# Kernel optimization log

Hardware: AMD Instinct MI355X
Metric: run time of the kernel (lower is better)

## Reference

```python
import jax, jax.numpy as jnp
import numpy as np

NEG_INF = -1e32

def _linear(x, W, b):
    # torch nn.Linear: x @ W.T + b
    return x @ W.T + b

def setup_inputs() -> dict:
    key = jax.random.key(0)
    B, T, D, H = 8, 1024, 512, 8
    ks = jax.random.split(key, 16)
    def rn(i, shape, scale=1.0):
        return jax.random.normal(ks[i], shape, dtype=jnp.float32) * scale
    W_SCALE = 0.04  # ~xavier for 512x512
    inp = {
        'q_mean': rn(0, (B, T, D)), 'q_cov': rn(1, (B, T, D)),
        'k_mean': rn(2, (B, T, D)), 'k_cov': rn(3, (B, T, D)),
        'v_mean': rn(4, (B, T, D)), 'v_cov': rn(5, (B, T, D)),
        # kq_same=True: q projections share k weights
        'Wk_mean': rn(6, (D, D), W_SCALE), 'bk_mean': jnp.zeros((D,), jnp.float32),
        'Wk_cov':  rn(7, (D, D), W_SCALE), 'bk_cov':  jnp.zeros((D,), jnp.float32),
        'Wv_mean': rn(8, (D, D), W_SCALE), 'bv_mean': jnp.zeros((D,), jnp.float32),
        'Wv_cov':  rn(9, (D, D), W_SCALE), 'bv_cov':  jnp.zeros((D,), jnp.float32),
        'Wo_mean': rn(10, (D, D), W_SCALE), 'bo_mean': jnp.zeros((D,), jnp.float32),
        'Wo_cov':  rn(11, (D, D), W_SCALE), 'bo_cov':  jnp.zeros((D,), jnp.float32),
        'gammas': rn(12, (H, 1, 1), 0.3),
        'mask': jnp.broadcast_to(jnp.tril(jnp.ones((T, T), dtype=bool))[None, None], (B, 1, T, T)),
        'zero_pad': 1,
    }
    return inp

def reference(q_mean, q_cov, k_mean, k_cov, v_mean, v_cov,
              Wk_mean, bk_mean, Wk_cov, bk_cov,
              Wv_mean, bv_mean, Wv_cov, bv_cov,
              Wo_mean, bo_mean, Wo_cov, bo_cov,
              gammas, mask, zero_pad):
    B, T, D = q_mean.shape
    H = gammas.shape[0]
    dk = D // H
    def split(x):  # (B,T,D) -> (B,H,T,dk)
        return x.reshape(B, T, H, dk).transpose(0, 2, 1, 3)
    km = split(_linear(k_mean, Wk_mean, bk_mean))
    kc = split(_linear(k_cov,  Wk_cov,  bk_cov))
    qm = split(_linear(q_mean, Wk_mean, bk_mean))  # kq_same
    qc = split(_linear(q_cov,  Wk_cov,  bk_cov))
    vm = split(_linear(v_mean, Wv_mean, bv_mean))
    vc = split(_linear(v_cov,  Wv_cov,  bv_cov))

    # Wasserstein distance (B,H,T,T)
    m1sq = jnp.sum(qm ** 2, -1, keepdims=True)
    m2sq = jnp.sum(km ** 2, -1, keepdims=True)
    ret = -2.0 * jnp.einsum('bhtd,bhsd->bhts', qm, km) + m1sq + jnp.swapaxes(m2sq, -1, -2)
    sq_q = jnp.sqrt(jnp.clip(qc, 1e-24))
    sq_k = jnp.sqrt(jnp.clip(kc, 1e-24))
    cov_ret = (-2.0 * jnp.einsum('bhtd,bhsd->bhts', sq_q, sq_k)
               + jnp.sum(qc, -1, keepdims=True)
               + jnp.swapaxes(jnp.sum(kc, -1, keepdims=True), -1, -2))
    scores = -(ret + cov_ret) / jnp.sqrt(jnp.float32(dk))

    # cumulative position-decay term (no-grad block in torch)
    s_ = jnp.where(mask, scores, NEG_INF)
    s_ = jax.nn.softmax(s_, axis=-1) * mask.astype(scores.dtype)
    distcum = jnp.cumsum(s_, axis=-1)
    disttot = jnp.sum(s_, axis=-1, keepdims=True)
    idx = jnp.arange(T)
    pos = jnp.abs(idx[None, :] - idx[:, None]).astype(jnp.float32)[None, None]  # (1,1,T,T)
    dist_scores = jax.lax.stop_gradient(jnp.sqrt(jnp.clip((disttot - distcum) * pos, 0.0)))

    gamma = -jax.nn.softplus(gammas)[None]  # (1,H,1,1)
    total_effect = jnp.clip(jnp.exp(dist_scores * gamma), 1e-5, 1e5)
    scores = jnp.where(mask, scores * total_effect, NEG_INF)
    scores = jax.nn.softmax(scores, axis=-1)
    if zero_pad:
        scores = scores.at[:, :, 0, :].set(0.0)
    # dropout is identity (p=0 / eval)

    out_mean = jnp.einsum('bhts,bhsd->bhtd', scores, vm)
    out_cov  = jnp.einsum('bhts,bhsd->bhtd', scores ** 2, vc)
    cm = out_mean.transpose(0, 2, 1, 3).reshape(B, T, D)
    cc = out_cov.transpose(0, 2, 1, 3).reshape(B, T, D)
    return (_linear(cm, Wo_mean, bo_mean), _linear(cc, Wo_cov, bo_cov))
```

## Files before the change

### kernel.cpp

```cpp
#include <hip/hip_runtime.h>
#include <hip/hip_bf16.h>
#include <hip/hip_fp16.h>

#define Bb 8
#define Tt 1024
#define Dd 512
#define Hh 8

typedef _Float16 half8 __attribute__((ext_vector_type(8)));
typedef float floatx4 __attribute__((ext_vector_type(4)));

__device__ __forceinline__ half8 cvt8(float4 a, float4 b) {
    half8 h;
    h[0] = (_Float16)a.x; h[1] = (_Float16)a.y; h[2] = (_Float16)a.z; h[3] = (_Float16)a.w;
    h[4] = (_Float16)b.x; h[5] = (_Float16)b.y; h[6] = (_Float16)b.z; h[7] = (_Float16)b.w;
    return h;
}

__device__ __forceinline__ void async16(const _Float16* g, _Float16* l) {
    __builtin_amdgcn_global_load_lds(
        (const __attribute__((address_space(1))) uint32_t*)g,
        (__attribute__((address_space(3))) uint32_t*)l, 16, 0, 0);
}

#define DPP_ADD(v, ctrl) \
    ((v) + __int_as_float(__builtin_amdgcn_update_dpp(0, __float_as_int(v), (ctrl), 0xF, 0xF, true)))

__device__ __forceinline__ float red16(float v) {
    v = DPP_ADD(v, 0xB1);
    v = DPP_ADD(v, 0x4E);
    v = DPP_ADD(v, 0x141);
    v = DPP_ADD(v, 0x140);
    return v;
}
__device__ __forceinline__ float scan16(float v) {
    v = DPP_ADD(v, 0x111);
    v = DPP_ADD(v, 0x112);
    v = DPP_ADD(v, 0x114);
    v = DPP_ADD(v, 0x118);
    return v;
}

template<bool TR>
__device__ __forceinline__ void gemm_tile(
    const float* __restrict__ X, const float* __restrict__ W,
    _Float16* As, _Float16* Bs, int m0, int n0, floatx4 acc[8])
{
    const int tid = threadIdx.x;
    const int w = tid >> 6, lane = tid & 63;
    const int sl = lane & 15, quad = lane >> 4;

    for (int k0 = 0; k0 < 512; k0 += 64) {
        __syncthreads();
        {
            const int r = tid >> 2;
            const int cb = (tid & 3) * 16;
            const float* xp = X + (size_t)(m0 + r) * 512 + k0 + cb;
            #pragma unroll
            for (int i = 0; i < 2; i++) {
                float4 v0 = *(const float4*)(xp + i * 8);
                float4 v1 = *(const float4*)(xp + i * 8 + 4);
                *(half8*)(As + r * 72 + cb + i * 8) = cvt8(v0, v1);
            }
        }
        {
            const int r = tid >> 1;
            const int cb = (tid & 1) * 32;
            const float* wp = W + (size_t)(n0 + r) * 512 + k0 + cb;
            #pragma unroll
            for (int i = 0; i < 4; i++) {
                float4 v0 = *(const float4*)(wp + i * 8);
                float4 v1 = *(const float4*)(wp + i * 8 + 4);
                *(half8*)(Bs + r * 72 + cb + i * 8) = cvt8(v0, v1);
            }
        }
        __syncthreads();
        #pragma unroll
        for (int kc = 0; kc < 64; kc += 32) {
            const half8 af = *(const half8*)(As + (w * 16 + sl) * 72 + kc + quad * 8);
            #pragma unroll
            for (int tn = 0; tn < 8; tn++) {
                const half8 bf = *(const half8*)(Bs + (tn * 16 + sl) * 72 + kc + quad * 8);
                if constexpr (TR)
                    acc[tn] = __builtin_amdgcn_mfma_f32_16x16x32_f16(bf, af, acc[tn], 0, 0, 0);
                else
                    acc[tn] = __builtin_amdgcn_mfma_f32_16x16x32_f16(af, bf, acc[tn], 0, 0, 0);
            }
        }
    }
}

__global__ __launch_bounds__(256) void gemm6(
    const float* __restrict__ q_mean, const float* __restrict__ q_cov,
    const float* __restrict__ k_mean, const float* __restrict__ k_cov,
    const float* __restrict__ v_mean, const float* __restrict__ v_cov,
    const float* __restrict__ Wk_mean, const float* __restrict__ bk_mean,
    const float* __restrict__ Wk_cov,  const float* __restrict__ bk_cov,
    const float* __restrict__ Wv_mean, const float* __restrict__ bv_mean,
    const float* __restrict__ Wv_cov,  const float* __restrict__ bv_cov,
    _Float16* __restrict__ QB, _Float16* __restrict__ KB, _Float16* __restrict__ VB,
    float* __restrict__ RROW, float* __restrict__ CCOL)
{
    __shared__ __align__(16) _Float16 As[64 * 72];
    __shared__ __align__(16) _Float16 Bs[128 * 72];

    const int f = blockIdx.x;
    const int work = (f & 7) * 384 + (f >> 3);
    const int z = work >> 9;
    const int rem = work & 511;
    const int m0 = (rem >> 2) * 64;
    const int n0 = (rem & 3) * 128;

    const float *X, *W, *bias; _Float16* outH; float* sums;
    int off, sumsq, do_sqrt;
    switch (z) {
    case 0:  X=q_mean; W=Wk_mean; bias=bk_mean; outH=QB; sums=RROW;   off=0;  sumsq=1; do_sqrt=0; break;
    case 1:  X=q_cov;  W=Wk_cov;  bias=bk_cov;  outH=QB; sums=RROW;   off=64; sumsq=0; do_sqrt=1; break;
    case 2:  X=k_mean; W=Wk_mean; bias=bk_mean; outH=KB; sums=CCOL;   off=0;  sumsq=1; do_sqrt=0; break;
    case 3:  X=k_cov;  W=Wk_cov;  bias=bk_cov;  outH=KB; sums=CCOL;   off=64; sumsq=0; do_sqrt=1; break;
    case 4:  X=v_mean; W=Wv_mean; bias=bv_mean; outH=VB; sums=nullptr;off=0;  sumsq=0; do_sqrt=0; break;
    default: X=v_cov;  W=Wv_cov;  bias=bv_cov;  outH=VB; sums=nullptr;off=64; sumsq=0; do_sqrt=0; break;
    }

    floatx4 acc[8];
    #pragma unroll
    for (int tn = 0; tn < 8; tn++) acc[tn] = (floatx4){0.f, 0.f, 0.f, 0.f};

    const int tid = threadIdx.x;
    const int w = tid >> 6, lane = tid & 63;
    const int sl = lane & 15, quad = lane >> 4;

    if (z < 4) {
        gemm_tile<false>(X, W, As, Bs, m0, n0, acc);
        #pragma unroll
        for (int r = 0; r < 4; r++) {
            const int m = m0 + w * 16 + quad * 4 + r;
            const int b = m >> 10, t = m & 1023;
            float rs0 = 0.f, rs1 = 0.f;
            #pragma unroll
            for (int tn = 0; tn < 8; tn++) {
                const int n = n0 + tn * 16 + sl;
                const float v = acc[tn][r] + bias[n];
                if (tn < 4) rs0 += sumsq ? v * v : v;
                else        rs1 += sumsq ? v * v : v;
                const float sv = do_sqrt ? sqrtf(fmaxf(v, 1e-24f)) : v;
                const int head = n >> 6, dd = n & 63;
                outH[(((size_t)b * Hh + head) * Tt + t) * 128 + off + dd] = (_Float16)sv;
            }
            if (sums) {
                float v0 = rs0, v1 = rs1;
                v0 += __shfl_xor(v0, 1); v0 += __shfl_xor(v0, 2);
                v0 += __shfl_xor(v0, 4); v0 += __shfl_xor(v0, 8);
                v1 += __shfl_xor(v1, 1); v1 += __shfl_xor(v1, 2);
                v1 += __shfl_xor(v1, 4); v1 += __shfl_xor(v1, 8);
                if (sl == 0) {
                    atomicAdd(&sums[((size_t)b * Hh + (n0 >> 6) + 0) * Tt + t], v0);
                    atomicAdd(&sums[((size_t)b * Hh + (n0 >> 6) + 1) * Tt + t], v1);
                }
            }
        }
    } else {
        gemm_tile<true>(X, W, As, Bs, m0, n0, acc);
        const int m = m0 + w * 16 + sl;
        const int b = m >> 10, t = m & 1023;
        #pragma unroll
        for (int r = 0; r < 4; r++) {
            #pragma unroll
            for (int tn = 0; tn < 8; tn++) {
                const int n = n0 + tn * 16 + quad * 4 + r;
                const float v = acc[tn][r] + bias[n];
                const int head = n >> 6, dd = n & 63;
                outH[(((size_t)b * Hh + head) * 128 + off + dd) * 1024 + t] = (_Float16)v;
            }
        }
    }
}

__global__ __launch_bounds__(256) void gemm_out(
    const float* __restrict__ CM, const float* __restrict__ CC,
    const float* __restrict__ Wo_mean, const float* __restrict__ bo_mean,
    const float* __restrict__ Wo_cov,  const float* __restrict__ bo_cov,
    float* __restrict__ out, size_t outStride)
{
    __shared__ __align__(16) _Float16 As[64 * 72];
    __shared__ __align__(16) _Float16 Bs[128 * 72];

    const int f = blockIdx.x;
    const int work = (f & 7) * 128 + (f >> 3);
    const int z = work >> 9;
    const int rem = work & 511;
    const int m0 = (rem >> 2) * 64;
    const int n0 = (rem & 3) * 128;

    const float* X    = z ? CC      : CM;
    const float* W    = z ? Wo_cov  : Wo_mean;
    const float* bias = z ? bo_cov  : bo_mean;
    float* outF       = out + (size_t)z * outStride;

    floatx4 acc[8];
    #pragma unroll
    for (int tn = 0; tn < 8; tn++) acc[tn] = (floatx4){0.f, 0.f, 0.f, 0.f};
    gemm_tile<false>(X, W, As, Bs, m0, n0, acc);

    const int tid = threadIdx.x;
    const int w = tid >> 6, lane = tid & 63;
    const int sl = lane & 15, quad = lane >> 4;

    #pragma unroll
    for (int r = 0; r < 4; r++) {
        const int m = m0 + w * 16 + quad * 4 + r;
        #pragma unroll
        for (int tn = 0; tn < 8; tn++) {
            const int n = n0 + tn * 16 + sl;
            outF[(size_t)m * 512 + n] = acc[tn][r] + bias[n];
        }
    }
}

__global__ __launch_bounds__(256) void attn_kernel(
    const _Float16* __restrict__ QB, const _Float16* __restrict__ KB,
    const _Float16* __restrict__ VBt, const float* __restrict__ RROW,
    const float* __restrict__ CCOL, const float* __restrict__ gammas,
    const int* __restrict__ zp, float* __restrict__ CM, float* __restrict__ CC)
{
    __shared__ __align__(16) _Float16 Vt[2][128 * 64];
    __shared__ __align__(16) _Float16 Pm[4][16 * 64];

    const int tid = threadIdx.x;
    const int g = blockIdx.x >> 6;
    const int bh = blockIdx.x & 63;
    const int rt = (g < 8) ? (15 - g) : (g - 8);
    const int t0 = rt * 64;
    const int h = bh & 7, b = bh >> 3;
    const int w = tid >> 6, lane = tid & 63;
    const int sl = lane & 15, quad = lane >> 4;
    const size_t rowbase = (size_t)bh * Tt;
    const int nch = rt + 1;

    const _Float16* VBb = VBt + (size_t)bh * 128 * 1024;
    const int vr8 = tid >> 3;
    const int vc8 = (tid & 7) << 3;
    const int vswz = (vr8 & 7) << 3;
    const _Float16* vsrc0 = VBb + (size_t)vr8 * 1024 + (vc8 ^ vswz);
    #define STAGE_V(cc, buf) do {                                          \
        const _Float16* _s = vsrc0 + (cc) * 64;                            \
        _Float16* _d = &Vt[(buf)][0] + vr8 * 64 + vc8;                     \
        _Pragma("unroll")                                                  \
        for (int _i = 0; _i < 4; _i++)                                     \
            async16(_s + (size_t)_i * 32 * 1024, _d + _i * 32 * 64);       \
    } while (0)

    STAGE_V(0, 0);

    half8 af[4];
    {
        const _Float16* qrow = QB + (rowbase + t0 + w * 16 + sl) * 128;
        #pragma unroll
        for (int ks = 0; ks < 4; ks++)
            af[ks] = *(const half8*)(qrow + ks * 32 + quad * 8);
    }

    const float gamma = -log1pf(__expf(gammas[h]));
    const int zero_pad = *zp;
    const int tbase = t0 + w * 16 + quad * 4;

    float rt_[4];
    #pragma unroll
    for (int r = 0; r < 4; r++) rt_[r] = RROW[rowbase + tbase + r];

    const _Float16* KBb = KB + rowbase * 128;
    const float* CCb = CCOL + rowbase;

    float l1p[4] = {0.f, 0.f, 0.f, 0.f};
    for (int c = 0; c < nch; ++c) {
        #pragma unroll
        for (int su = 0; su < 4; su++) {
            const int scol = c * 64 + su * 16 + sl;
            const _Float16* kr = KBb + (size_t)scol * 128;
            floatx4 acc = {0.f, 0.f, 0.f, 0.f};
            #pragma unroll
            for (int ks = 0; ks < 4; ks++) {
                half8 bf = *(const half8*)(kr + ks * 32 + quad * 8);
                acc = __builtin_amdgcn_mfma_f32_16x16x32_f16(af[ks], bf, acc, 0, 0, 0);
            }
            const float cs = CCb[scol];
            #pragma unroll
            for (int r = 0; r < 4; r++) {
                const float S = 0.25f * acc[r] - 0.125f * (rt_[r] + cs);
                l1p[r] += (scol <= tbase + r) ? __expf(S) : 0.f;
            }
        }
    }
    float invl1[4];
    #pragma unroll
    for (int r = 0; r < 4; r++) invl1[r] = 1.f / red16(l1p[r]);

    __syncthreads();

    float cumc[4] = {0.f, 0.f, 0.f, 0.f};
    float runL2[4] = {0.f, 0.f, 0.f, 0.f};
    floatx4 accm[4], accc[4];
    #pragma unroll
    for (int nt = 0; nt < 4; nt++) {
        accm[nt] = (floatx4){0.f, 0.f, 0.f, 0.f};
        accc[nt] = (floatx4){0.f, 0.f, 0.f, 0.f};
    }
    _Float16* PmW = &Pm[w][0];

    for (int c = 0; c < nch; ++c) {
        const int cur = c & 1;
        if (c + 1 < nch) STAGE_V(c + 1, cur ^ 1);

        float p2v[4][4];
        float csum[4] = {0.f, 0.f, 0.f, 0.f};
        #pragma unroll
        for (int su = 0; su < 4; su++) {
            const int scol = c * 64 + su * 16 + sl;
            const _Float16* kr = KBb + (size_t)scol * 128;
            floatx4 acc = {0.f, 0.f, 0.f, 0.f};
            #pragma unroll
            for (int ks = 0; ks < 4; ks++) {
                half8 bf = *(const half8*)(kr + ks * 32 + quad * 8);
                acc = __builtin_amdgcn_mfma_f32_16x16x32_f16(af[ks], bf, acc, 0, 0, 0);
            }
            const float cs = CCb[scol];
            #pragma unroll
            for (int r = 0; r < 4; r++) {
                const bool valid = (scol <= tbase + r);
                const float S = 0.25f * acc[r] - 0.125f * (rt_[r] + cs);
                const float p1 = valid ? __expf(S) : 0.f;
                const float cum = cumc[r] + scan16(p1);
                cumc[r] += red16(p1);
                const float sn = 1.f - cum * invl1[r];
                const float dsq = sn * (float)(tbase + r - scol);
                const float dist = sqrtf(fmaxf(dsq, 0.f));
                float dec = __expf(gamma * dist);
                dec = fminf(fmaxf(dec, 1e-5f), 1e5f);
                const float p2 = valid ? __expf(S * dec) : 0.f;
                p2v[su][r] = p2;
                csum[r] += p2;
            }
        }

        float invL2c[4];
        #pragma unroll
        for (int r = 0; r < 4; r++) {
            const float v = red16(csum[r]);
            const float newL2 = runL2[r] + v;
            const float inv = 1.f / newL2;
            const float ratio = runL2[r] * inv;
            runL2[r] = newL2;
            invL2c[r] = inv;
            const float ratio2 = ratio * ratio;
            #pragma unroll
            for (int nt = 0; nt < 4; nt++) {
                accm[nt][r] *= ratio;
                accc[nt][r] *= ratio2;
            }
        }
        #pragma unroll
        for (int su = 0; su < 4; su++) {
            #pragma unroll
            for (int r = 0; r < 4; r++) {
                const float pn = p2v[su][r] * invL2c[r];
                const int prow = quad * 4 + r;
                PmW[prow * 64 + ((su * 16 + sl) ^ ((prow & 7) << 3))] = (_Float16)pn;
            }
        }

        const _Float16* Vc = &Vt[cur][0];
        #pragma unroll
        for (int ks = 0; ks < 2; ks++) {
            const int kb = ks * 32 + quad * 8;
            half8 am = *(const half8*)(PmW + sl * 64 + (kb ^ ((sl & 7) << 3)));
            half8 ac = am * am;
            #pragma unroll
            for (int nt = 0; nt < 4; nt++) {
                const int rm = nt * 16 + sl, rc = rm + 64;
                half8 bm = *(const half8*)(Vc + rm * 64 + (kb ^ ((rm & 7) << 3)));
                half8 bc = *(const half8*)(Vc + rc * 64 + (kb ^ ((rc & 7) << 3)));
                accm[nt] = __builtin_amdgcn_mfma_f32_16x16x32_f16(am, bm, accm[nt], 0, 0, 0);
                accc[nt] = __builtin_amdgcn_mfma_f32_16x16x32_f16(ac, bc, accc[nt], 0, 0, 0);
            }
        }
        __syncthreads();
    }

    #pragma unroll
    for (int r = 0; r < 4; r++) {
        const int t = tbase + r;
        const bool zr = (zero_pad && t == 0);
        float* cmp = CM + ((size_t)b * Tt + t) * Dd + h * 64;
        float* ccp = CC + ((size_t)b * Tt + t) * Dd + h * 64;
        #pragma unroll
        for (int nt = 0; nt < 4; nt++) {
            const int d = nt * 16 + sl;
            cmp[d] = zr ? 0.f : accm[nt][r];
            ccp[d] = zr ? 0.f : accc[nt][r];
        }
    }
    #undef STAGE_V
}

extern "C" void kernel_launch(void* const* d_in, const int* in_sizes, int n_in,
                              void* d_out, int out_size, void* d_ws, size_t ws_size,
                              hipStream_t stream)
{
    const float* q_mean  = (const float*)d_in[0];
    const float* q_cov   = (const float*)d_in[1];
    const float* k_mean  = (const float*)d_in[2];
    const float* k_cov   = (const float*)d_in[3];
    const float* v_mean  = (const float*)d_in[4];
    const float* v_cov   = (const float*)d_in[5];
    const float* Wk_mean = (const float*)d_in[6];
    const float* bk_mean = (const float*)d_in[7];
    const float* Wk_cov  = (const float*)d_in[8];
    const float* bk_cov  = (const float*)d_in[9];
    const float* Wv_mean = (const float*)d_in[10];
    const float* bv_mean = (const float*)d_in[11];
    const float* Wv_cov  = (const float*)d_in[12];
    const float* bv_cov  = (const float*)d_in[13];
    const float* Wo_mean = (const float*)d_in[14];
    const float* bo_mean = (const float*)d_in[15];
    const float* Wo_cov  = (const float*)d_in[16];
    const float* bo_cov  = (const float*)d_in[17];
    const float* gammas  = (const float*)d_in[18];
    const int* zero_pad  = (const int*)d_in[20];
    float* out = (float*)d_out;

    const size_t N_BHT128 = (size_t)Bb * Hh * Tt * 128;
    const size_t N_BHT    = (size_t)Bb * Hh * Tt;
    const size_t N_BTD    = (size_t)Bb * Tt * Dd;
    const size_t needed = 3 * N_BHT128 * sizeof(_Float16)
                        + (2 * N_BHT + 2 * N_BTD) * sizeof(float);
    if (ws_size < needed) return;

    _Float16* QB = (_Float16*)d_ws;
    _Float16* KB = QB + N_BHT128;
    _Float16* VB = KB + N_BHT128;
    float* RROW = (float*)(VB + N_BHT128);
    float* CCOL = RROW + N_BHT;
    float* CM   = CCOL + N_BHT;
    float* CC   = CM + N_BTD;

    hipMemsetAsync(RROW, 0, 2 * N_BHT * sizeof(float), stream);

    gemm6<<<dim3(3072), dim3(256), 0, stream>>>(
        q_mean, q_cov, k_mean, k_cov, v_mean, v_cov,
        Wk_mean, bk_mean, Wk_cov, bk_cov,
        Wv_mean, bv_mean, Wv_cov, bv_cov,
        QB, KB, VB, RROW, CCOL);

    attn_kernel<<<dim3(1024), dim3(256), 0, stream>>>(
        QB, KB, VB, RROW, CCOL, gammas, zero_pad, CM, CC);

    gemm_out<<<dim3(1024), dim3(256), 0, stream>>>(
        CM, CC, Wo_mean, bo_mean, Wo_cov, bo_cov, out, N_BTD);
}
```

Baseline: 535.5 us.

## Pre-convert inputs and weights to fp16 and store attention outputs in fp16

Adds a pre-pass kernel that converts all six fp32 activations and six weight matrices to fp16 in workspace. The projection and output GEMMs then load fp16 tiles directly instead of reloading fp32 and converting per tile. The attention kernel writes its intermediate outputs in fp16, halving that round trip. This trades an extra full read/write pass over the inputs for less repeated fp32 traffic and conversion work, with some added precision loss on intermediates.

```diff
diff --git a/kernel.cpp b/kernel.cpp
--- a/kernel.cpp
+++ b/kernel.cpp
@@ -41,9 +41,45 @@
     return v;
 }
 
+__global__ __launch_bounds__(256) void cvt_pre(
+    const float* __restrict__ s0, const float* __restrict__ s1,
+    const float* __restrict__ s2, const float* __restrict__ s3,
+    const float* __restrict__ s4, const float* __restrict__ s5,
+    const float* __restrict__ w0, const float* __restrict__ w1,
+    const float* __restrict__ w2, const float* __restrict__ w3,
+    const float* __restrict__ w4, const float* __restrict__ w5,
+    _Float16* __restrict__ dst)
+{
+    const size_t N_BTD = (size_t)Bb * Tt * Dd;
+    const size_t NX = 6 * N_BTD;
+    const size_t total8 = (NX + 6 * 262144) / 8;
+    size_t i = (size_t)blockIdx.x * 256 + threadIdx.x;
+    const size_t stride = (size_t)gridDim.x * 256;
+    for (; i < total8; i += stride) {
+        const size_t e = i * 8;
+        const float* src;
+        size_t off;
+        if (e < NX) {
+            const int seg = (int)(e >> 22);
+            off = e & (N_BTD - 1);
+            src = (seg == 0) ? s0 : (seg == 1) ? s1 : (seg == 2) ? s2
+                : (seg == 3) ? s3 : (seg == 4) ? s4 : s5;
+        } else {
+            const size_t we = e - NX;
+            const int seg = (int)(we >> 18);
+            off = we & 262143;
+            src = (seg == 0) ? w0 : (seg == 1) ? w1 : (seg == 2) ? w2
+                : (seg == 3) ? w3 : (seg == 4) ? w4 : w5;
+        }
+        float4 a = *(const float4*)(src + off);
+        float4 b = *(const float4*)(src + off + 4);
+        *(half8*)(dst + e) = cvt8(a, b);
+    }
+}
+
 template<bool TR>
-__device__ __forceinline__ void gemm_tile(
-    const float* __restrict__ X, const float* __restrict__ W,
+__device__ __forceinline__ void gemm_tile_h(
+    const _Float16* __restrict__ X, const _Float16* __restrict__ W,
     _Float16* As, _Float16* Bs, int m0, int n0, floatx4 acc[8])
 {
     const int tid = threadIdx.x;
@@ -55,24 +91,17 @@
         {
             const int r = tid >> 2;
             const int cb = (tid & 3) * 16;
-            const float* xp = X + (size_t)(m0 + r) * 512 + k0 + cb;
-            #pragma unroll
-            for (int i = 0; i < 2; i++) {
-                float4 v0 = *(const float4*)(xp + i * 8);
-                float4 v1 = *(const float4*)(xp + i * 8 + 4);
-                *(half8*)(As + r * 72 + cb + i * 8) = cvt8(v0, v1);
-            }
+            const _Float16* xp = X + (size_t)(m0 + r) * 512 + k0 + cb;
+            *(uint4*)(As + r * 72 + cb)     = *(const uint4*)(xp);
+            *(uint4*)(As + r * 72 + cb + 8) = *(const uint4*)(xp + 8);
         }
         {
             const int r = tid >> 1;
             const int cb = (tid & 1) * 32;
-            const float* wp = W + (size_t)(n0 + r) * 512 + k0 + cb;
-            #pragma unroll
-            for (int i = 0; i < 4; i++) {
-                float4 v0 = *(const float4*)(wp + i * 8);
-                float4 v1 = *(const float4*)(wp + i * 8 + 4);
-                *(half8*)(Bs + r * 72 + cb + i * 8) = cvt8(v0, v1);
-            }
+            const _Float16* wp = W + (size_t)(n0 + r) * 512 + k0 + cb;
+            #pragma unroll
+            for (int i = 0; i < 4; i++)
+                *(uint4*)(Bs + r * 72 + cb + i * 8) = *(const uint4*)(wp + i * 8);
         }
         __syncthreads();
         #pragma unroll
@@ -91,13 +120,9 @@
 }
 
 __global__ __launch_bounds__(256) void gemm6(
-    const float* __restrict__ q_mean, const float* __restrict__ q_cov,
-    const float* __restrict__ k_mean, const float* __restrict__ k_cov,
-    const float* __restrict__ v_mean, const float* __restrict__ v_cov,
-    const float* __restrict__ Wk_mean, const float* __restrict__ bk_mean,
-    const float* __restrict__ Wk_cov,  const float* __restrict__ bk_cov,
-    const float* __restrict__ Wv_mean, const float* __restrict__ bv_mean,
-    const float* __restrict__ Wv_cov,  const float* __restrict__ bv_cov,
+    const _Float16* __restrict__ XH, const _Float16* __restrict__ WH,
+    const float* __restrict__ bk_mean, const float* __restrict__ bk_cov,
+    const float* __restrict__ bv_mean, const float* __restrict__ bv_cov,
     _Float16* __restrict__ QB, _Float16* __restrict__ KB, _Float16* __restrict__ VB,
     float* __restrict__ RROW, float* __restrict__ CCOL)
 {
@@ -111,15 +136,19 @@
     const int m0 = (rem >> 2) * 64;
     const int n0 = (rem & 3) * 128;
 
-    const float *X, *W, *bias; _Float16* outH; float* sums;
+    const size_t N_BTD = (size_t)Bb * Tt * Dd;
+    const _Float16* X = XH + (size_t)z * N_BTD;
+    const _Float16* W;
+    const float* bias;
+    _Float16* outH; float* sums;
     int off, sumsq, do_sqrt;
     switch (z) {
-    case 0:  X=q_mean; W=Wk_mean; bias=bk_mean; outH=QB; sums=RROW;   off=0;  sumsq=1; do_sqrt=0; break;
-    case 1:  X=q_cov;  W=Wk_cov;  bias=bk_cov;  outH=QB; sums=RROW;   off=64; sumsq=0; do_sqrt=1; break;
-    case 2:  X=k_mean; W=Wk_mean; bias=bk_mean; outH=KB; sums=CCOL;   off=0;  sumsq=1; do_sqrt=0; break;
-    case 3:  X=k_cov;  W=Wk_cov;  bias=bk_cov;  outH=KB; sums=CCOL;   off=64; sumsq=0; do_sqrt=1; break;
-    case 4:  X=v_mean; W=Wv_mean; bias=bv_mean; outH=VB; sums=nullptr;off=0;  sumsq=0; do_sqrt=0; break;
-    default: X=v_cov;  W=Wv_cov;  bias=bv_cov;  outH=VB; sums=nullptr;off=64; sumsq=0; do_sqrt=0; break;
+    case 0:  W=WH;            bias=bk_mean; outH=QB; sums=RROW;   off=0;  sumsq=1; do_sqrt=0; break;
+    case 1:  W=WH+262144;     bias=bk_cov;  outH=QB; sums=RROW;   off=64; sumsq=0; do_sqrt=1; break;
+    case 2:  W=WH;            bias=bk_mean; outH=KB; sums=CCOL;   off=0;  sumsq=1; do_sqrt=0; break;
+    case 3:  W=WH+262144;     bias=bk_cov;  outH=KB; sums=CCOL;   off=64; sumsq=0; do_sqrt=1; break;
+    case 4:  W=WH+2*262144;   bias=bv_mean; outH=VB; sums=nullptr;off=0;  sumsq=0; do_sqrt=0; break;
+    default: W=WH+3*262144;   bias=bv_cov;  outH=VB; sums=nullptr;off=64; sumsq=0; do_sqrt=0; break;
     }
 
     floatx4 acc[8];
@@ -131,7 +160,7 @@
     const int sl = lane & 15, quad = lane >> 4;
 
     if (z < 4) {
-        gemm_tile<false>(X, W, As, Bs, m0, n0, acc);
+        gemm_tile_h<false>(X, W, As, Bs, m0, n0, acc);
         #pragma unroll
         for (int r = 0; r < 4; r++) {
             const int m = m0 + w * 16 + quad * 4 + r;
@@ -160,7 +189,7 @@
             }
         }
     } else {
-        gemm_tile<true>(X, W, As, Bs, m0, n0, acc);
+        gemm_tile_h<true>(X, W, As, Bs, m0, n0, acc);
         const int m = m0 + w * 16 + sl;
         const int b = m >> 10, t = m & 1023;
         #pragma unroll
@@ -177,9 +206,9 @@
 }
 
 __global__ __launch_bounds__(256) void gemm_out(
-    const float* __restrict__ CM, const float* __restrict__ CC,
-    const float* __restrict__ Wo_mean, const float* __restrict__ bo_mean,
-    const float* __restrict__ Wo_cov,  const float* __restrict__ bo_cov,
+    const _Float16* __restrict__ CMh, const _Float16* __restrict__ CCh,
+    const _Float16* __restrict__ WH,
+    const float* __restrict__ bo_mean, const float* __restrict__ bo_cov,
     float* __restrict__ out, size_t outStride)
 {
     __shared__ __align__(16) _Float16 As[64 * 72];
@@ -192,15 +221,15 @@
     const int m0 = (rem >> 2) * 64;
     const int n0 = (rem & 3) * 128;
 
-    const float* X    = z ? CC      : CM;
-    const float* W    = z ? Wo_cov  : Wo_mean;
-    const float* bias = z ? bo_cov  : bo_mean;
+    const _Float16* X = z ? CCh : CMh;
+    const _Float16* W = WH + (size_t)(4 + z) * 262144;
+    const float* bias = z ? bo_cov : bo_mean;
     float* outF       = out + (size_t)z * outStride;
 
     floatx4 acc[8];
     #pragma unroll
     for (int tn = 0; tn < 8; tn++) acc[tn] = (floatx4){0.f, 0.f, 0.f, 0.f};
-    gemm_tile<false>(X, W, As, Bs, m0, n0, acc);
+    gemm_tile_h<false>(X, W, As, Bs, m0, n0, acc);
 
     const int tid = threadIdx.x;
     const int w = tid >> 6, lane = tid & 63;
@@ -221,7 +250,7 @@
     const _Float16* __restrict__ QB, const _Float16* __restrict__ KB,
     const _Float16* __restrict__ VBt, const float* __restrict__ RROW,
     const float* __restrict__ CCOL, const float* __restrict__ gammas,
-    const int* __restrict__ zp, float* __restrict__ CM, float* __restrict__ CC)
+    const int* __restrict__ zp, _Float16* __restrict__ CMh, _Float16* __restrict__ CCh)
 {
     __shared__ __align__(16) _Float16 Vt[2][128 * 64];
     __shared__ __align__(16) _Float16 Pm[4][16 * 64];
@@ -390,13 +419,13 @@
     for (int r = 0; r < 4; r++) {
         const int t = tbase + r;
         const bool zr = (zero_pad && t == 0);
-        float* cmp = CM + ((size_t)b * Tt + t) * Dd + h * 64;
-        float* ccp = CC + ((size_t)b * Tt + t) * Dd + h * 64;
+        _Float16* cmp = CMh + ((size_t)b * Tt + t) * Dd + h * 64;
+        _Float16* ccp = CCh + ((size_t)b * Tt + t) * Dd + h * 64;
         #pragma unroll
         for (int nt = 0; nt < 4; nt++) {
             const int d = nt * 16 + sl;
-            cmp[d] = zr ? 0.f : accm[nt][r];
-            ccp[d] = zr ? 0.f : accc[nt][r];
+            cmp[d] = (_Float16)(zr ? 0.f : accm[nt][r]);
+            ccp[d] = (_Float16)(zr ? 0.f : accc[nt][r]);
         }
     }
     #undef STAGE_V
@@ -431,29 +460,36 @@
     const size_t N_BHT128 = (size_t)Bb * Hh * Tt * 128;
     const size_t N_BHT    = (size_t)Bb * Hh * Tt;
     const size_t N_BTD    = (size_t)Bb * Tt * Dd;
+
     const size_t needed = 3 * N_BHT128 * sizeof(_Float16)
-                        + (2 * N_BHT + 2 * N_BTD) * sizeof(float);
+                        + 6 * N_BTD * sizeof(_Float16)
+                        + 6 * 262144 * sizeof(_Float16)
+                        + 2 * N_BHT * sizeof(float);
     if (ws_size < needed) return;
 
     _Float16* QB = (_Float16*)d_ws;
     _Float16* KB = QB + N_BHT128;
     _Float16* VB = KB + N_BHT128;
-    float* RROW = (float*)(VB + N_BHT128);
+    _Float16* XH = VB + N_BHT128;
+    _Float16* WH = XH + 6 * N_BTD;
+    float* RROW = (float*)(WH + 6 * 262144);
     float* CCOL = RROW + N_BHT;
-    float* CM   = CCOL + N_BHT;
-    float* CC   = CM + N_BTD;
+    _Float16* CMh = XH;
+    _Float16* CCh = CMh + N_BTD;
 
     hipMemsetAsync(RROW, 0, 2 * N_BHT * sizeof(float), stream);
 
+    cvt_pre<<<dim3(2048), dim3(256), 0, stream>>>(
+        q_mean, q_cov, k_mean, k_cov, v_mean, v_cov,
+        Wk_mean, Wk_cov, Wv_mean, Wv_cov, Wo_mean, Wo_cov, XH);
+
     gemm6<<<dim3(3072), dim3(256), 0, stream>>>(
-        q_mean, q_cov, k_mean, k_cov, v_mean, v_cov,
-        Wk_mean, bk_mean, Wk_cov, bk_cov,
-        Wv_mean, bv_mean, Wv_cov, bv_cov,
+        XH, WH, bk_mean, bk_cov, bv_mean, bv_cov,
         QB, KB, VB, RROW, CCOL);
 
     attn_kernel<<<dim3(1024), dim3(256), 0, stream>>>(
-        QB, KB, VB, RROW, CCOL, gammas, zero_pad, CM, CC);
+        QB, KB, VB, RROW, CCOL, gammas, zero_pad, CMh, CCh);
 
     gemm_out<<<dim3(1024), dim3(256), 0, stream>>>(
-        CM, CC, Wo_mean, bo_mean, Wo_cov, bo_cov, out, N_BTD);
-}
+        CMh, CCh, WH, bo_mean, bo_cov, out, N_BTD);
+}
```

New measurement: 482.4 us. 9.9% less time.
